# Performance work log

Hardware: AMD Instinct MI355X
Metric: run time of the kernel (lower is better)

## Reference

```python
import jax, jax.numpy as jnp
import numpy as np

N_BLOCKS = 2
N_LAYERS = 14
N_HIDDEN = 128
N_CLASSES = 256
BATCH = 4
T = 64000
DIMS = ('NCH', 'OIH', 'NCH')


def setup_inputs() -> dict:
    key = jax.random.key(0)
    ks = jax.random.split(key, 5)
    seq = jax.random.normal(ks[0], (BATCH, 1, T), dtype=jnp.float32)
    # xavier-uniform-like scales
    s_first = float(np.sqrt(6.0 / (1 * 2 + N_HIDDEN * 2)))
    s_rest = float(np.sqrt(6.0 / (N_HIDDEN * 2 + N_HIDDEN * 2)))
    s_cls = float(np.sqrt(6.0 / (N_HIDDEN + N_CLASSES)))
    w_first = jax.random.uniform(ks[1], (N_HIDDEN, 1, 2), jnp.float32, -s_first, s_first)
    w_rest = jax.random.uniform(ks[2], (N_BLOCKS * N_LAYERS - 1, N_HIDDEN, N_HIDDEN, 2), jnp.float32, -s_rest, s_rest)
    w_cls = jax.random.uniform(ks[3], (N_CLASSES, N_HIDDEN), jnp.float32, -s_cls, s_cls)
    b_cls = jnp.full((N_CLASSES,), 0.001, dtype=jnp.float32)
    return {"seq": seq, "w_first": w_first, "w_rest": w_rest, "w_cls": w_cls, "b_cls": b_cls}


def reference(seq, w_first, w_rest, w_cls, b_cls):
    x = seq  # [N, 1, T]
    for i in range(N_BLOCKS * N_LAYERS):
        l = i % N_LAYERS
        d = 2 ** (l % 10)  # dilation cycles 1..512
        W = w_first if i == 0 else w_rest[i - 1]
        # causal pad by d on the left, dilated conv with kernel size 2, then ReLU
        x = jax.lax.conv_general_dilated(
            x, W, window_strides=(1,), padding=[(d, 0)],
            rhs_dilation=(d,), dimension_numbers=DIMS)
        x = jax.nn.relu(x)
    # 1x1 classifier conv: [N, n_hidden, T] -> [N, n_classes, T]
    out = jnp.einsum('oc,nct->not', w_cls, x) + b_cls[None, :, None]
    return out
```

## Files before the change

### kernel.cpp

```cpp
#include <hip/hip_runtime.h>
#include <hip/hip_bf16.h>

#define BATCH 4
#define T 64000
#define C 128
#define NCLS 256
#define NLAYER 28

typedef __attribute__((ext_vector_type(8))) short short8;
typedef __attribute__((ext_vector_type(4))) float f32x4;
typedef unsigned short u16;

static __device__ __forceinline__ u16 f2bf(float x) {
    __hip_bfloat16 h = __float2bfloat16(x);
    return *reinterpret_cast<u16*>(&h);
}

__global__ void prep_weights(const float* __restrict__ w_rest,
                             const float* __restrict__ w_cls,
                             u16* __restrict__ Wt, u16* __restrict__ Wc)
{
    const size_t n1 = (size_t)27 * 128 * 256;
    const size_t n2 = (size_t)NCLS * C;
    for (size_t idx = (size_t)blockIdx.x * 256 + threadIdx.x; idx < n1 + n2;
         idx += (size_t)gridDim.x * 256) {
        if (idx < n1) {
            const int k   = (int)(idx & 255);
            const int o   = (int)((idx >> 8) & 127);
            const int l   = (int)(idx >> 15);
            const int tap = k >> 7;
            const int i   = k & 127;
            Wt[idx] = f2bf(w_rest[(((size_t)l * 128 + o) * 128 + i) * 2 + tap]);
        } else {
            const size_t j = idx - n1;
            Wc[j] = f2bf(w_cls[j]);
        }
    }
}

__global__ void first_layer(const float* __restrict__ seq,
                            u16* __restrict__ xout,
                            const float* __restrict__ wf)
{
    __shared__ float w0[C], w1[C];
    const int tid = threadIdx.x;
    if (tid < C) { w0[tid] = wf[tid * 2]; w1[tid] = wf[tid * 2 + 1]; }
    __syncthreads();

    const int b  = blockIdx.y;
    const int og = tid & 15;
#pragma unroll
    for (int tt = 0; tt < 4; ++tt) {
        const int t = blockIdx.x * 64 + tt * 16 + (tid >> 4);
        const float s1 = seq[(size_t)b * T + t];
        const float s0 = (t > 0) ? seq[(size_t)b * T + t - 1] : 0.f;
        short8 v = {};
#pragma unroll
        for (int k = 0; k < 8; ++k) {
            const int o = og * 8 + k;
            float y = fmaf(w0[o], s0, w1[o] * s1);
            y = y > 0.f ? y : 0.f;
            v[k] = (short)f2bf(y);
        }
        *reinterpret_cast<short8*>(xout + ((size_t)b * T + t) * C + og * 8) = v;
    }
}

__global__ __launch_bounds__(512, 2) void conv_layer(
    const u16* __restrict__ xin, u16* __restrict__ xout,
    const u16* __restrict__ Wt, int d)
{
    __shared__ u16 wlds[C * 256];
    const int tid = threadIdx.x;
#pragma unroll
    for (int c = 0; c < 8; ++c) {
        const int cc = c * 512 + tid;
        const int o = cc >> 5, kc = cc & 31;
        short8 v = *reinterpret_cast<const short8*>(Wt + o * 256 + kc * 8);
        *reinterpret_cast<short8*>(&wlds[o * 256 + ((kc * 8) ^ ((o & 7) << 3))]) = v;
    }
    __syncthreads();

    const int b    = blockIdx.y;
    const int wv   = tid >> 6, lane = tid & 63;
    const int wr   = wv >> 1, wc = wv & 1;
    const int l15  = lane & 15, l4 = lane >> 4;
    const u16* xb  = xin  + (size_t)b * T * C;
    u16*       yb  = xout + (size_t)b * T * C;

    for (int it = 0; it < 4; ++it) {
        const int t0 = (blockIdx.x * 4 + it) * 128;
        f32x4 acc[2][4] = {};

#pragma unroll
        for (int tap = 0; tap < 2; ++tap) {
#pragma unroll
            for (int k0 = 0; k0 < 128; k0 += 32) {
                short8 af[2];
#pragma unroll
                for (int a = 0; a < 2; ++a) {
                    const int trow = t0 + wr * 32 + a * 16 + l15 - (tap ? 0 : d);
                    const int ch   = k0 + l4 * 8;
                    short8 v = {};
                    if (trow >= 0)
                        v = *reinterpret_cast<const short8*>(xb + (size_t)trow * C + ch);
                    af[a] = v;
                }
                const int koff = tap * 128 + k0 + l4 * 8;
#pragma unroll
                for (int j = 0; j < 4; ++j) {
                    const int o = wc * 64 + j * 16 + l15;
                    short8 bf = *reinterpret_cast<const short8*>(
                        &wlds[o * 256 + (koff ^ ((o & 7) << 3))]);
                    acc[0][j] = __builtin_amdgcn_mfma_f32_16x16x32_bf16(af[0], bf, acc[0][j], 0, 0, 0);
                    acc[1][j] = __builtin_amdgcn_mfma_f32_16x16x32_bf16(af[1], bf, acc[1][j], 0, 0, 0);
                }
            }
        }
#pragma unroll
        for (int a = 0; a < 2; ++a) {
#pragma unroll
            for (int r = 0; r < 4; ++r) {
                const int t = t0 + wr * 32 + a * 16 + l4 * 4 + r;
#pragma unroll
                for (int j = 0; j < 4; ++j) {
                    const int o = wc * 64 + j * 16 + l15;
                    float y = acc[a][j][r];
                    y = y > 0.f ? y : 0.f;
                    yb[(size_t)t * C + o] = f2bf(y);
                }
            }
        }
    }
}

__global__ __launch_bounds__(512, 2) void cls_layer(
    const u16* __restrict__ xin, float* __restrict__ out,
    const u16* __restrict__ Wc, const float* __restrict__ bias)
{
    __shared__ u16 wlds[NCLS * C];
    const int tid = threadIdx.x;
#pragma unroll
    for (int c = 0; c < 8; ++c) {
        const int cc = c * 512 + tid;
        const int o = cc >> 4, kc = cc & 15;
        short8 v = *reinterpret_cast<const short8*>(Wc + o * C + kc * 8);
        *reinterpret_cast<short8*>(&wlds[o * C + ((kc * 8) ^ ((o & 7) << 3))]) = v;
    }
    __syncthreads();

    const int b   = blockIdx.y;
    const int wv  = tid >> 6, lane = tid & 63;
    const int wr  = wv >> 2, wc = wv & 3;
    const int l15 = lane & 15, l4 = lane >> 4;
    const u16* xb = xin + (size_t)b * T * C;
    float*     ob = out + (size_t)b * NCLS * T;

    for (int it = 0; it < 8; ++it) {
        const int t0 = (blockIdx.x * 8 + it) * 64;
        f32x4 acc[2][4] = {};

#pragma unroll
        for (int k0 = 0; k0 < 128; k0 += 32) {
            short8 af[2];
#pragma unroll
            for (int a = 0; a < 2; ++a) {
                const int trow = t0 + wr * 32 + a * 16 + l15;
                af[a] = *reinterpret_cast<const short8*>(xb + (size_t)trow * C + k0 + l4 * 8);
            }
            const int koff = k0 + l4 * 8;
#pragma unroll
            for (int j = 0; j < 4; ++j) {
                const int o = wc * 64 + j * 16 + l15;
                short8 bf = *reinterpret_cast<const short8*>(
                    &wlds[o * C + (koff ^ ((o & 7) << 3))]);
                acc[0][j] = __builtin_amdgcn_mfma_f32_16x16x32_bf16(af[0], bf, acc[0][j], 0, 0, 0);
                acc[1][j] = __builtin_amdgcn_mfma_f32_16x16x32_bf16(af[1], bf, acc[1][j], 0, 0, 0);
            }
        }
#pragma unroll
        for (int a = 0; a < 2; ++a) {
#pragma unroll
            for (int j = 0; j < 4; ++j) {
                const int o = wc * 64 + j * 16 + l15;
                const int t = t0 + wr * 32 + a * 16 + l4 * 4;
                const float bs = bias[o];
                f32x4 v = acc[a][j];
                float4 w = make_float4(v[0] + bs, v[1] + bs, v[2] + bs, v[3] + bs);
                *reinterpret_cast<float4*>(ob + (size_t)o * T + t) = w;
            }
        }
    }
}

extern "C" void kernel_launch(void* const* d_in, const int* in_sizes, int n_in,
                              void* d_out, int out_size, void* d_ws, size_t ws_size,
                              hipStream_t stream)
{
    const float* seq   = (const float*)d_in[0];
    const float* wf    = (const float*)d_in[1];
    const float* wrest = (const float*)d_in[2];
    const float* wcls  = (const float*)d_in[3];
    const float* bcls  = (const float*)d_in[4];
    float* out = (float*)d_out;

    const size_t xElems  = (size_t)BATCH * T * C;
    const size_t wtElems = (size_t)27 * 128 * 256;
    const size_t wcElems = (size_t)NCLS * C;

    u16 *xA, *xB, *Wt, *Wc;
    if (ws_size >= (2 * xElems + wtElems + wcElems + 1024) * sizeof(u16)) {
        xA = (u16*)d_ws;
        xB = xA + xElems;
        Wt = xB + xElems;
    } else {
        xA = (u16*)d_out;
        xB = (u16*)d_ws;
        Wt = xB + xElems;
    }
    Wc = Wt + wtElems;

    prep_weights<<<dim3(896), dim3(256), 0, stream>>>(wrest, wcls, Wt, Wc);
    first_layer<<<dim3(T / 64, BATCH), dim3(256), 0, stream>>>(seq, xA, wf);

    u16* cur = xA;
    u16* nxt = xB;
    for (int i = 1; i < NLAYER; ++i) {
        const int d = 1 << ((i % 14) % 10);
        conv_layer<<<dim3(T / 512, BATCH), dim3(512), 0, stream>>>(
            cur, nxt, Wt + (size_t)(i - 1) * 128 * 256, d);
        u16* tmp = cur; cur = nxt; nxt = tmp;
    }
    cls_layer<<<dim3(T / 512, BATCH), dim3(512), 0, stream>>>(cur, out, Wc, bcls);
}
```

Before: 1.470 ms.

## Fuse all dilated conv layers into one persistent cooperative kernel with grid sync

Replaces the 27 per-layer conv launches with a single cooperative persistent kernel of 512 blocks of 256 threads. Each block reloads the layer's weights into LDS, then loops over 64-timestep tiles across all batches, and the grid synchronises between layers. The goal is to remove launch gaps and per-layer tail effects, and to amortise each weight load over more tiles. In exchange it runs fewer waves per CU, which may weaken latency hiding, and it adds the cost of a grid-wide barrier per layer.

```diff
diff --git a/kernel.cpp b/kernel.cpp
--- a/kernel.cpp
+++ b/kernel.cpp
@@ -1,5 +1,8 @@
 #include <hip/hip_runtime.h>
 #include <hip/hip_bf16.h>
+#include <hip/hip_cooperative_groups.h>
+
+namespace cg = cooperative_groups;
 
 #define BATCH 4
 #define T 64000
@@ -66,71 +69,80 @@
     }
 }
 
-__global__ __launch_bounds__(512, 2) void conv_layer(
-    const u16* __restrict__ xin, u16* __restrict__ xout,
-    const u16* __restrict__ Wt, int d)
-{
+__global__ __launch_bounds__(256, 2) void conv_all(
+    u16* __restrict__ xA, u16* __restrict__ xB, const u16* __restrict__ Wt)
+{
+    cg::grid_group grid = cg::this_grid();
     __shared__ u16 wlds[C * 256];
     const int tid = threadIdx.x;
-#pragma unroll
-    for (int c = 0; c < 8; ++c) {
-        const int cc = c * 512 + tid;
-        const int o = cc >> 5, kc = cc & 31;
-        short8 v = *reinterpret_cast<const short8*>(Wt + o * 256 + kc * 8);
-        *reinterpret_cast<short8*>(&wlds[o * 256 + ((kc * 8) ^ ((o & 7) << 3))]) = v;
-    }
-    __syncthreads();
-
-    const int b    = blockIdx.y;
-    const int wv   = tid >> 6, lane = tid & 63;
-    const int wr   = wv >> 1, wc = wv & 1;
-    const int l15  = lane & 15, l4 = lane >> 4;
-    const u16* xb  = xin  + (size_t)b * T * C;
-    u16*       yb  = xout + (size_t)b * T * C;
-
-    for (int it = 0; it < 4; ++it) {
-        const int t0 = (blockIdx.x * 4 + it) * 128;
-        f32x4 acc[2][4] = {};
-
-#pragma unroll
-        for (int tap = 0; tap < 2; ++tap) {
-#pragma unroll
-            for (int k0 = 0; k0 < 128; k0 += 32) {
-                short8 af[2];
-#pragma unroll
-                for (int a = 0; a < 2; ++a) {
-                    const int trow = t0 + wr * 32 + a * 16 + l15 - (tap ? 0 : d);
-                    const int ch   = k0 + l4 * 8;
-                    short8 v = {};
-                    if (trow >= 0)
-                        v = *reinterpret_cast<const short8*>(xb + (size_t)trow * C + ch);
-                    af[a] = v;
+    const int wv  = tid >> 6, lane = tid & 63;
+    const int wr  = wv >> 1, wc = wv & 1;
+    const int l15 = lane & 15, l4 = lane >> 4;
+
+    u16* bufs[2] = { xA, xB };
+
+    for (int i = 1; i < NLAYER; ++i) {
+        const int d = 1 << ((i % 14) % 10);
+        const u16* W   = Wt + (size_t)(i - 1) * (C * 256);
+        const u16* cur = bufs[(i - 1) & 1];
+        u16*       nxt = bufs[i & 1];
+
+#pragma unroll
+        for (int c = 0; c < 16; ++c) {
+            const int cc = c * 256 + tid;
+            const int o = cc >> 5, kc = cc & 31;
+            short8 v = *reinterpret_cast<const short8*>(W + o * 256 + kc * 8);
+            *reinterpret_cast<short8*>(&wlds[o * 256 + ((kc * 8) ^ ((o & 7) << 3))]) = v;
+        }
+        __syncthreads();
+
+        for (int tl = blockIdx.x; tl < 4000; tl += gridDim.x) {
+            const int b  = tl / 1000;
+            const int t0 = (tl - b * 1000) * 64;
+            const u16* xb = cur + (size_t)b * T * C;
+            u16*       yb = nxt + (size_t)b * T * C;
+
+            f32x4 acc[2][4] = {};
+#pragma unroll
+            for (int tap = 0; tap < 2; ++tap) {
+#pragma unroll
+                for (int k0 = 0; k0 < 128; k0 += 32) {
+                    short8 af[2];
+#pragma unroll
+                    for (int a = 0; a < 2; ++a) {
+                        const int trow = t0 + wr * 32 + a * 16 + l15 - (tap ? 0 : d);
+                        short8 v = {};
+                        if (trow >= 0)
+                            v = *reinterpret_cast<const short8*>(
+                                    xb + (size_t)trow * C + k0 + l4 * 8);
+                        af[a] = v;
+                    }
+                    const int koff = tap * 128 + k0 + l4 * 8;
+#pragma unroll
+                    for (int j = 0; j < 4; ++j) {
+                        const int o = wc * 64 + j * 16 + l15;
+                        short8 bf = *reinterpret_cast<const short8*>(
+                            &wlds[o * 256 + (koff ^ ((o & 7) << 3))]);
+                        acc[0][j] = __builtin_amdgcn_mfma_f32_16x16x32_bf16(af[0], bf, acc[0][j], 0, 0, 0);
+                        acc[1][j] = __builtin_amdgcn_mfma_f32_16x16x32_bf16(af[1], bf, acc[1][j], 0, 0, 0);
+                    }
                 }
-                const int koff = tap * 128 + k0 + l4 * 8;
-#pragma unroll
-                for (int j = 0; j < 4; ++j) {
-                    const int o = wc * 64 + j * 16 + l15;
-                    short8 bf = *reinterpret_cast<const short8*>(
-                        &wlds[o * 256 + (koff ^ ((o & 7) << 3))]);
-                    acc[0][j] = __builtin_amdgcn_mfma_f32_16x16x32_bf16(af[0], bf, acc[0][j], 0, 0, 0);
-                    acc[1][j] = __builtin_amdgcn_mfma_f32_16x16x32_bf16(af[1], bf, acc[1][j], 0, 0, 0);
+            }
+#pragma unroll
+            for (int a = 0; a < 2; ++a) {
+#pragma unroll
+                for (int r = 0; r < 4; ++r) {
+                    const int t = t0 + wr * 32 + a * 16 + l4 * 4 + r;
+#pragma unroll
+                    for (int j = 0; j < 4; ++j) {
+                        const int o = wc * 64 + j * 16 + l15;
+                        float y = acc[a][j][r];
+                        yb[(size_t)t * C + o] = f2bf(y > 0.f ? y : 0.f);
+                    }
                 }
             }
         }
-#pragma unroll
-        for (int a = 0; a < 2; ++a) {
-#pragma unroll
-            for (int r = 0; r < 4; ++r) {
-                const int t = t0 + wr * 32 + a * 16 + l4 * 4 + r;
-#pragma unroll
-                for (int j = 0; j < 4; ++j) {
-                    const int o = wc * 64 + j * 16 + l15;
-                    float y = acc[a][j][r];
-                    y = y > 0.f ? y : 0.f;
-                    yb[(size_t)t * C + o] = f2bf(y);
-                }
-            }
-        }
+        grid.sync();
     }
 }
 
@@ -206,10 +218,9 @@
 
     const size_t xElems  = (size_t)BATCH * T * C;
     const size_t wtElems = (size_t)27 * 128 * 256;
-    const size_t wcElems = (size_t)NCLS * C;
 
     u16 *xA, *xB, *Wt, *Wc;
-    if (ws_size >= (2 * xElems + wtElems + wcElems + 1024) * sizeof(u16)) {
+    if (ws_size >= (2 * xElems + wtElems + (size_t)NCLS * C + 1024) * sizeof(u16)) {
         xA = (u16*)d_ws;
         xB = xA + xElems;
         Wt = xB + xElems;
@@ -223,13 +234,9 @@
     prep_weights<<<dim3(896), dim3(256), 0, stream>>>(wrest, wcls, Wt, Wc);
     first_layer<<<dim3(T / 64, BATCH), dim3(256), 0, stream>>>(seq, xA, wf);
 
-    u16* cur = xA;
-    u16* nxt = xB;
-    for (int i = 1; i < NLAYER; ++i) {
-        const int d = 1 << ((i % 14) % 10);
-        conv_layer<<<dim3(T / 512, BATCH), dim3(512), 0, stream>>>(
-            cur, nxt, Wt + (size_t)(i - 1) * 128 * 256, d);
-        u16* tmp = cur; cur = nxt; nxt = tmp;
-    }
-    cls_layer<<<dim3(T / 512, BATCH), dim3(512), 0, stream>>>(cur, out, Wc, bcls);
-}
+    void* cargs[] = { (void*)&xA, (void*)&xB, (void*)&Wt };
+    hipLaunchCooperativeKernel((void*)conv_all, dim3(512), dim3(256),
+                               cargs, 0, stream);
+
+    cls_layer<<<dim3(T / 512, BATCH), dim3(512), 0, stream>>>(xB, out, Wc, bcls);
+}
```

New measurement: 3.234 ms. +119.9%, slower.
